# Optimization experiments

Hardware: AMD Instinct MI355X
Metric: run time of the kernel (lower is better)

The kernel has to match this reference:

```python
import jax, jax.numpy as jnp
import numpy as np

B, N, EMB = 64, 2048, 128
K1 = 3
L = EMB - K1 + 1            # 126, width after conv1/conv2
K2 = L // 2 + 1             # 64, conv3 kernel width -> conv3 out width = K2 - 1 = 63


def _conv_relu(x, w, b):
    # x: [M, 1, H, W]; w: [O, 1, kh, kw]; VALID conv + bias + relu
    y = jax.lax.conv_general_dilated(
        x, w, window_strides=(1, 1), padding='VALID',
        dimension_numbers=('NCHW', 'OIHW', 'NCHW'))
    return jax.nn.relu(y + b[None, :, None, None])


def _score(pairs, W1, b1, W2, b2, W3, b3, fw1, fb1, fw2, fb2, fw3, fb3):
    # pairs: [M, 2, D] -> score [M]
    x = pairs[:, None]                                  # [M,1,2,D]
    c1 = _conv_relu(x, W1, b1)                          # [M,1,2,L]
    c2 = _conv_relu(x, W2, b2)                          # [M,1,1,L]
    c = jnp.concatenate([c1, c2], axis=2)               # [M,1,3,L]
    c3 = _conv_relu(c, W3, b3)                          # [M,1,1,K2-1]
    h = c3.reshape(c3.shape[0], -1)                     # [M,K2-1]
    h = h @ fw1.T + fb1                                 # [M,K2//4]
    h = h @ fw2.T + fb2                                 # [M,16]
    h = h @ fw3.T + fb3                                 # [M,1]
    return h[:, 0]


def setup_inputs() -> dict:
    key = jax.random.key(0)
    ks = jax.random.split(key, 12)
    users = jax.random.normal(ks[0], (B, N, EMB), jnp.float32)
    top_user = jax.random.normal(ks[1], (B, EMB), jnp.float32)
    question = jax.random.normal(ks[2], (B, EMB), jnp.float32)
    # ragged valid-lengths: uids nonzero for first `len` entries, zero after
    lengths = jax.random.randint(ks[3], (B,), 1, N + 1)
    vals = jax.random.randint(ks[4], (B, N), 1, 10000)
    uids = jnp.where(jnp.arange(N)[None, :] < lengths[:, None], vals, 0).astype(jnp.int64)
    s = 0.1
    return {
        'users': users, 'top_user': top_user, 'question': question, 'uids': uids,
        'W1': jax.random.normal(ks[5], (1, 1, 1, K1), jnp.float32) * s,
        'b1': jnp.zeros((1,), jnp.float32),
        'W2': jax.random.normal(ks[6], (1, 1, 2, K1), jnp.float32) * s,
        'b2': jnp.zeros((1,), jnp.float32),
        'W3': jax.random.normal(ks[7], (1, 1, 3, K2), jnp.float32) * s,
        'b3': jnp.zeros((1,), jnp.float32),
        'fw1': jax.random.normal(ks[8], (K2 // 4, K2 - 1), jnp.float32) * s,
        'fb1': jnp.zeros((K2 // 4,), jnp.float32),
        'fw2': jax.random.normal(ks[9], (16, K2 // 4), jnp.float32) * s,
        'fb2': jnp.zeros((16,), jnp.float32),
        'fw3': jax.random.normal(ks[10], (1, 16), jnp.float32) * s,
        'fb3': jnp.zeros((1,), jnp.float32),
    }


def reference(users, top_user, question, uids,
              W1, b1, W2, b2, W3, b3, fw1, fb1, fw2, fb2, fw3, fb3):
    b, n, d = users.shape
    params = (W1, b1, W2, b2, W3, b3, fw1, fb1, fw2, fb2, fw3, fb3)
    # low-rank pairs: (candidate user, question) for every candidate slot
    q = jnp.broadcast_to(question[:, None], (b, n, d))
    low = jnp.stack([users, q], axis=2).reshape(b * n, 2, d)      # [B*N,2,D]
    high = jnp.stack([top_user, question], axis=1)                # [B,2,D]
    low_s = _score(low, *params).reshape(b, n)                    # [B,N]
    high_s = _score(high, *params)                                # [B]
    # ragged length = index of first zero uid (torch loop breaks there)
    is_zero = uids == 0
    cnt = jnp.where(jnp.any(is_zero, axis=1), jnp.argmax(is_zero, axis=1), n)
    mask = (jnp.arange(n)[None, :] < cnt[:, None]).astype(low_s.dtype)
    return jnp.sum(jax.nn.sigmoid(low_s - high_s[:, None]) * mask)
```

## Files before the change

### kernel.cpp

```cpp
#include <hip/hip_runtime.h>
#include <hip/hip_bf16.h>

typedef __attribute__((ext_vector_type(8))) short short8v;
typedef __attribute__((ext_vector_type(4))) float float4v;

#define NB 64
#define NN 2048
#define ED 128
#define GRID_P 1024

#define WS_WEFF  0
#define WS_BEFF  64
#define WS_SHIGH 128
#define WS_QTERM 192
#define WS_QPRE  (192+4096)
#define WS_BPACK (192+4096+8192)

static __device__ __forceinline__ unsigned int packbf2(float a, float b) {
    __hip_bfloat162 h = __float22bfloat162_rn(make_float2(a, b));
    return *(unsigned int*)&h;
}

__global__ __launch_bounds__(64) void k_prep(
    const float* __restrict__ top_user, const float* __restrict__ question,
    const float* __restrict__ W1, const float* __restrict__ b1,
    const float* __restrict__ W2, const float* __restrict__ b2,
    const float* __restrict__ W3, const float* __restrict__ b3,
    const float* __restrict__ fw1, const float* __restrict__ fb1,
    const float* __restrict__ fw2, const float* __restrict__ fb2,
    const float* __restrict__ fw3, const float* __restrict__ fb3,
    float* __restrict__ ws, float* __restrict__ out)
{
    const int lane = threadIdx.x;
    const int blk = blockIdx.x;
    __shared__ float g[16];
    __shared__ float w3s[192];
    w3s[lane] = W3[lane];
    w3s[64 + lane] = W3[64 + lane];
    w3s[128 + lane] = W3[128 + lane];
    if (lane < 16) {
        float s = 0.f;
        #pragma unroll
        for (int i = 0; i < 16; ++i) s += fw3[i] * fw2[i*16 + lane];
        g[lane] = s;
    }
    __syncthreads();

    if (blk >= NB) {
        const int kt = blk - NB;
        if (kt == 0) {
            if (lane == 0) out[0] = 0.f;
            float wv = 0.f;
            if (lane < 63) {
                #pragma unroll
                for (int k = 0; k < 16; ++k) wv += g[k] * fw1[k*63 + lane];
            }
            ws[WS_WEFF + lane] = wv;
            if (lane == 0) {
                float be = fb3[0];
                #pragma unroll
                for (int i = 0; i < 16; ++i) be += fw3[i] * fb2[i];
                #pragma unroll
                for (int k = 0; k < 16; ++k) be += g[k] * fb1[k];
                ws[WS_BEFF] = be;
            }
        }
        __hip_bfloat16* bp = (__hip_bfloat16*)(ws + WS_BPACK);
        const int g8 = (lane >> 4) * 8, li = lane & 15;
        #pragma unroll
        for (int nt = 0; nt < 4; ++nt) {
            const int tt = nt*16 + li;
            #pragma unroll
            for (int idx = 0; idx < 8; ++idx) {
                const int k = kt*32 + g8 + idx;
                const int j = k - tt;
                const int k2 = k - 128, j2 = k2 - tt;
                const bool v0 = (tt < 63) && (k < 126) && (j >= 0) && (j < 64);
                const bool v2 = (tt < 63) && (k2 >= 0) && (k2 < 126) && (j2 >= 0) && (j2 < 64);
                float v = (v0 ? w3s[j & 63] : 0.f) + (v2 ? w3s[128 + (j2 & 63)] : 0.f);
                bp[((kt*4 + nt)*64 + lane)*8 + idx] = __float2bfloat16(v);
            }
        }
        return;
    }

    float wv = 0.f;
    if (lane < 63) {
        #pragma unroll
        for (int k = 0; k < 16; ++k) wv += g[k] * fw1[k*63 + lane];
    }
    float be = fb3[0];
    #pragma unroll
    for (int i = 0; i < 16; ++i) be += fw3[i] * fb2[i];
    #pragma unroll
    for (int k = 0; k < 16; ++k) be += g[k] * fb1[k];

    __shared__ float q[132], tu[132], c1q[128], qt[64];
    __shared__ float4 D4[64];
    const int b = blk;
    ((float2*)q)[lane]  = ((const float2*)(question + b*ED))[lane];
    ((float2*)tu)[lane] = ((const float2*)(top_user + b*ED))[lane];
    if (lane == 63) {
        q[128]=0.f; q[129]=0.f; q[130]=0.f; q[131]=0.f;
        tu[128]=0.f; tu[129]=0.f; tu[130]=0.f; tu[131]=0.f;
    }
    __syncthreads();
    const float w10=W1[0], w11=W1[1], w12=W1[2];
    const float w20=W2[0], w21=W2[1], w22=W2[2];
    const float w23=W2[3], w24=W2[4], w25=W2[5];
    const float b1v=b1[0], b2v=b2[0], b3v=b3[0];
    const int i = 2*lane;
    float c1qa = fmaxf(b1v + w10*q[i]   + w11*q[i+1] + w12*q[i+2], 0.f);
    float c1qb = fmaxf(b1v + w10*q[i+1] + w11*q[i+2] + w12*q[i+3], 0.f);
    float qpa  = w23*q[i]   + w24*q[i+1] + w25*q[i+2];
    float qpb  = w23*q[i+1] + w24*q[i+2] + w25*q[i+3];
    float c1ta = fmaxf(b1v + w10*tu[i]   + w11*tu[i+1] + w12*tu[i+2], 0.f);
    float c1tb = fmaxf(b1v + w10*tu[i+1] + w11*tu[i+2] + w12*tu[i+3], 0.f);
    float c2a  = fmaxf(b2v + w20*tu[i]   + w21*tu[i+1] + w22*tu[i+2] + qpa, 0.f);
    float c2b  = fmaxf(b2v + w20*tu[i+1] + w21*tu[i+2] + w22*tu[i+3] + qpb, 0.f);
    if (lane == 63) { c1qa=0.f; c1qb=0.f; qpa=0.f; qpb=0.f; c1ta=0.f; c1tb=0.f; c2a=0.f; c2b=0.f; }
    c1q[i] = c1qa; c1q[i+1] = c1qb;
    ws[WS_QPRE + b*128 + i]     = qpa;
    ws[WS_QPRE + b*128 + i + 1] = qpb;
    D4[lane] = make_float4(c1ta, c2a, c1tb, c2b);
    __syncthreads();
    float qtv = 0.f;
    if (lane < 63) {
        #pragma unroll
        for (int j = 0; j < 64; ++j) qtv += w3s[64 + j] * c1q[lane + j];
    }
    qt[lane] = qtv;
    ws[WS_QTERM + b*64 + lane] = qtv + b3v;
    __syncthreads();
    float acc0 = b3v + qt[lane];
    float acc1 = 0.f;
    const float2* D2 = (const float2*)D4;
    #pragma unroll
    for (int j = 0; j < 64; ++j) {
        const float2 d = D2[lane + j];
        acc0 = fmaf(w3s[j],       d.x, acc0);
        acc1 = fmaf(w3s[128 + j], d.y, acc1);
    }
    float v = wv * fmaxf(acc0 + acc1, 0.f);
    #pragma unroll
    for (int off = 32; off > 0; off >>= 1) v += __shfl_xor(v, off, 64);
    if (lane == 0) ws[WS_SHIGH + b] = v + be;
}

__global__ __launch_bounds__(256) void k_pairs(
    const float* __restrict__ users, const int* __restrict__ uids,
    float* __restrict__ ws, float* __restrict__ out,
    const float* __restrict__ W1, const float* __restrict__ b1,
    const float* __restrict__ W2, const float* __restrict__ b2)
{
    __shared__ __align__(16) unsigned int X[64][132];
    __shared__ float pscore[2][2][64];
    const int tid = threadIdx.x;
    const int w = tid >> 6, lane = tid & 63;
    const int bid = blockIdx.x;
    const int b = bid >> 4;
    const int cpair = bid & 15;
    const int base0 = b*NN + cpair*128;
    const int base1 = base0 + 64;

    if (uids[base0] == 0) return;
    const bool act1 = (uids[base1] != 0);

    const int g = lane >> 4, li = lane & 15;
    const int nhalf = w >> 1;
    const int mbase = (w & 1) * 32;

    const int myuid0 = (w == 0) ? uids[base0 + lane] : 1;
    const int myuid1 = (w == 0) ? uids[base1 + lane] : 1;

    const float w10=W1[0], w11=W1[1], w12=W1[2];
    const float w20=W2[0], w21=W2[1], w22=W2[2];
    const float b1v=b1[0], b2v=b2[0];
    const int h = lane >> 5, j = lane & 31;
    const int r0 = w * 16;

    float4 u0r[8], u1r[8];
    #pragma unroll
    for (int pass = 0; pass < 8; ++pass) {
        const int r = r0 + pass*2 + h;
        u0r[pass] = *(const float4*)(users + (size_t)(base0 + r)*ED + 4*j);
        u1r[pass] = *(const float4*)(users + (size_t)(base1 + r)*ED + 4*j);
    }

    const __hip_bfloat16* bp = (const __hip_bfloat16*)(ws + WS_BPACK);
    short8v bfr0[8], bfr1[8];
    #pragma unroll
    for (int kt = 0; kt < 8; ++kt) {
        bfr0[kt] = *(const short8v*)(bp + (((kt*4 + nhalf*2 + 0)*64 + lane) << 3));
        bfr1[kt] = *(const short8v*)(bp + (((kt*4 + nhalf*2 + 1)*64 + lane) << 3));
    }

    const int t0 = nhalf*32 + li, t1 = t0 + 16;
    const float wf0 = ws[WS_WEFF + t0], wf1 = ws[WS_WEFF + t1];
    const float qt0 = ws[WS_QTERM + b*64 + t0], qt1 = ws[WS_QTERM + b*64 + t1];
    const float shigh = ws[WS_SHIGH + b], beff = ws[WS_BEFF];
    const float4 qp4 = *(const float4*)&ws[WS_QPRE + b*128 + 4*j];

    auto prep = [&](const float4* ur) {
        #pragma unroll
        for (int pass = 0; pass < 8; ++pass) {
            const int r = r0 + pass*2 + h;
            const float4 uu = ur[pass];
            const float nx = __shfl(uu.x, (lane + 1) & 63, 64);
            const float ny = __shfl(uu.y, (lane + 1) & 63, 64);
            float c10 = fmaxf(b1v + w10*uu.x + w11*uu.y + w12*uu.z, 0.f);
            float c11 = fmaxf(b1v + w10*uu.y + w11*uu.z + w12*uu.w, 0.f);
            float c12 = fmaxf(b1v + w10*uu.z + w11*uu.w + w12*nx  , 0.f);
            float c13 = fmaxf(b1v + w10*uu.w + w11*nx   + w12*ny  , 0.f);
            float c20 = fmaxf(b2v + w20*uu.x + w21*uu.y + w22*uu.z + qp4.x, 0.f);
            float c21 = fmaxf(b2v + w20*uu.y + w21*uu.z + w22*uu.w + qp4.y, 0.f);
            float c22 = fmaxf(b2v + w20*uu.z + w21*uu.w + w22*nx   + qp4.z, 0.f);
            float c23 = fmaxf(b2v + w20*uu.w + w21*nx   + w22*ny   + qp4.w, 0.f);
            if (j == 31) { c12 = 0.f; c13 = 0.f; c22 = 0.f; c23 = 0.f; }
            uint2 v1; v1.x = packbf2(c10, c11); v1.y = packbf2(c12, c13);
            uint2 v2; v2.x = packbf2(c20, c21); v2.y = packbf2(c22, c23);
            *(uint2*)&X[r][2*j]      = v1;
            *(uint2*)&X[r][64 + 2*j] = v2;
        }
    };

    auto gemm_ep = [&](int c) {
        float4v acc00 = {0.f,0.f,0.f,0.f}, acc01 = {0.f,0.f,0.f,0.f};
        float4v acc10 = {0.f,0.f,0.f,0.f}, acc11 = {0.f,0.f,0.f,0.f};
        const char* Xb = (const char*)&X[0][0];
        #pragma unroll
        for (int kt = 0; kt < 8; ++kt) {
            const short8v a0 = *(const short8v*)(Xb + (mbase + li)*528      + kt*64 + g*16);
            const short8v a1 = *(const short8v*)(Xb + (mbase + 16 + li)*528 + kt*64 + g*16);
            acc00 = __builtin_amdgcn_mfma_f32_16x16x32_bf16(a0, bfr0[kt], acc00, 0, 0, 0);
            acc01 = __builtin_amdgcn_mfma_f32_16x16x32_bf16(a0, bfr1[kt], acc01, 0, 0, 0);
            acc10 = __builtin_amdgcn_mfma_f32_16x16x32_bf16(a1, bfr0[kt], acc10, 0, 0, 0);
            acc11 = __builtin_amdgcn_mfma_f32_16x16x32_bf16(a1, bfr1[kt], acc11, 0, 0, 0);
        }
        #pragma unroll
        for (int mi = 0; mi < 2; ++mi) {
            #pragma unroll
            for (int reg = 0; reg < 4; ++reg) {
                const float a0v = mi ? acc10[reg] : acc00[reg];
                const float a1v = mi ? acc11[reg] : acc01[reg];
                float v = wf0 * fmaxf(a0v + qt0, 0.f) + wf1 * fmaxf(a1v + qt1, 0.f);
                v += __shfl_xor(v, 1, 64);
                v += __shfl_xor(v, 2, 64);
                v += __shfl_xor(v, 4, 64);
                v += __shfl_xor(v, 8, 64);
                if (li == 0) pscore[c][nhalf][mbase + mi*16 + g*4 + reg] = v;
            }
        }
    };

    prep(u0r);
    __syncthreads();
    gemm_ep(0);
    __syncthreads();
    if (act1) prep(u1r);
    __syncthreads();
    if (act1) gemm_ep(1);
    __syncthreads();

    if (w == 0) {
        const float d0 = pscore[0][0][lane] + pscore[0][1][lane] + beff - shigh;
        float val = (myuid0 != 0) ? 1.f / (1.f + __expf(-d0)) : 0.f;
        if (act1) {
            const float d1 = pscore[1][0][lane] + pscore[1][1][lane] + beff - shigh;
            val += (myuid1 != 0) ? 1.f / (1.f + __expf(-d1)) : 0.f;
        }
        #pragma unroll
        for (int off = 32; off > 0; off >>= 1) val += __shfl_xor(val, off, 64);
        if (lane == 0) atomicAdd(out, val);
    }
}

extern "C" void kernel_launch(void* const* d_in, const int* in_sizes, int n_in,
                              void* d_out, int out_size, void* d_ws, size_t ws_size,
                              hipStream_t stream)
{
    const float* users    = (const float*)d_in[0];
    const float* top_user = (const float*)d_in[1];
    const float* question = (const float*)d_in[2];
    const int*   uids     = (const int*)d_in[3];
    const float* W1  = (const float*)d_in[4];
    const float* b1  = (const float*)d_in[5];
    const float* W2  = (const float*)d_in[6];
    const float* b2  = (const float*)d_in[7];
    const float* W3  = (const float*)d_in[8];
    const float* b3  = (const float*)d_in[9];
    const float* fw1 = (const float*)d_in[10];
    const float* fb1 = (const float*)d_in[11];
    const float* fw2 = (const float*)d_in[12];
    const float* fb2 = (const float*)d_in[13];
    const float* fw3 = (const float*)d_in[14];
    const float* fb3 = (const float*)d_in[15];
    float* ws  = (float*)d_ws;
    float* out = (float*)d_out;

    hipLaunchKernelGGL(k_prep, dim3(NB + 8), dim3(64), 0, stream,
                       top_user, question, W1, b1, W2, b2, W3, b3,
                       fw1, fb1, fw2, fb2, fw3, fb3, ws, out);
    hipLaunchKernelGGL(k_pairs, dim3(GRID_P), dim3(256), 0, stream,
                       users, uids, ws, out, W1, b1, W2, b2);
}
```

Baseline: 31.74 us.

## Compact active 64-row chunks via prefix sum and launch one chunk per block

k_prep now counts, for each batch row, how many 64-candidate chunks begin with a nonzero uid and writes the counts to workspace. k_pairs runs a wave-level prefix scan over these counts, so each block maps to exactly one active chunk and inactive blocks exit early. This replaces the old fixed mapping of two chunks per block, which left blocks idle on padded rows and underused the GPU. The cost is a per-block scan over the 64 counts and a grid sized for the worst case, with excess blocks returning immediately.

```diff
diff --git a/kernel.cpp b/kernel.cpp
--- a/kernel.cpp
+++ b/kernel.cpp
@@ -7,7 +7,7 @@
 #define NB 64
 #define NN 2048
 #define ED 128
-#define GRID_P 1024
+#define GRID_P 2048
 
 #define WS_WEFF  0
 #define WS_BEFF  64
@@ -15,6 +15,7 @@
 #define WS_QTERM 192
 #define WS_QPRE  (192+4096)
 #define WS_BPACK (192+4096+8192)
+#define WS_QCNT  (WS_BPACK+8192)
 
 static __device__ __forceinline__ unsigned int packbf2(float a, float b) {
     __hip_bfloat162 h = __float22bfloat162_rn(make_float2(a, b));
@@ -29,10 +30,15 @@
     const float* __restrict__ fw1, const float* __restrict__ fb1,
     const float* __restrict__ fw2, const float* __restrict__ fb2,
     const float* __restrict__ fw3, const float* __restrict__ fb3,
+    const int* __restrict__ uids,
     float* __restrict__ ws, float* __restrict__ out)
 {
     const int lane = threadIdx.x;
     const int blk = blockIdx.x;
+
+    int act = 0;
+    if (blk < NB && lane < 32) act = (uids[blk*NN + lane*64] != 0) ? 1 : 0;
+
     __shared__ float g[16];
     __shared__ float w3s[192];
     w3s[lane] = W3[lane];
@@ -84,6 +90,11 @@
         return;
     }
 
+    {
+        const unsigned long long bm = __ballot(act);
+        if (lane == 0) ((int*)(ws + WS_QCNT))[blk] = (int)__popcll(bm);
+    }
+
     float wv = 0.f;
     if (lane < 63) {
         #pragma unroll
@@ -154,88 +165,93 @@
     const float* __restrict__ W2, const float* __restrict__ b2)
 {
     __shared__ __align__(16) unsigned int X[64][132];
-    __shared__ float pscore[2][2][64];
+    __shared__ float pscore[2][64];
     const int tid = threadIdx.x;
     const int w = tid >> 6, lane = tid & 63;
     const int bid = blockIdx.x;
-    const int b = bid >> 4;
-    const int cpair = bid & 15;
-    const int base0 = b*NN + cpair*128;
-    const int base1 = base0 + 64;
-
-    if (uids[base0] == 0) return;
-    const bool act1 = (uids[base1] != 0);
-
-    const int g = lane >> 4, li = lane & 15;
+
+    const int* qcnti = (const int*)(ws + WS_QCNT);
+    int incl = qcnti[lane];
+    #pragma unroll
+    for (int off = 1; off < 64; off <<= 1) {
+        const int t = __shfl_up(incl, off, 64);
+        if (lane >= off) incl += t;
+    }
+    const int total = __shfl(incl, 63, 64);
+    if (bid >= total) return;
+
+    const unsigned long long mm = __ballot(incl <= bid);
+    const int b0 = (int)__popcll(mm);
+    const int prefb = (b0 > 0) ? __shfl(incl, b0 - 1, 64) : 0;
+    const int pa0 = b0*NN + (bid - prefb)*64;
+
+    const int gfr = lane >> 4, li = lane & 15;
     const int nhalf = w >> 1;
     const int mbase = (w & 1) * 32;
-
-    const int myuid0 = (w == 0) ? uids[base0 + lane] : 1;
-    const int myuid1 = (w == 0) ? uids[base1 + lane] : 1;
+    const int h = lane >> 5, j = lane & 31;
+    const int r0 = w * 16;
+
+    float4 bufA[8];
+    #pragma unroll
+    for (int pass = 0; pass < 8; ++pass) {
+        const int r = r0 + pass*2 + h;
+        bufA[pass] = *(const float4*)(users + (size_t)(pa0 + r)*ED + 4*j);
+    }
+    const int m0 = (w == 0) ? uids[pa0 + lane] : 1;
+
+    const __hip_bfloat16* bp = (const __hip_bfloat16*)(ws + WS_BPACK);
+    short8v bfr0[8], bfr1[8];
+    #pragma unroll
+    for (int kt = 0; kt < 8; ++kt) {
+        bfr0[kt] = *(const short8v*)(bp + (((kt*4 + nhalf*2 + 0)*64 + lane) << 3));
+        bfr1[kt] = *(const short8v*)(bp + (((kt*4 + nhalf*2 + 1)*64 + lane) << 3));
+    }
+
+    const int t0 = nhalf*32 + li, t1 = t0 + 16;
+    const float wf0 = ws[WS_WEFF + t0], wf1 = ws[WS_WEFF + t1];
+    const float beff = ws[WS_BEFF];
+    const float qta0 = ws[WS_QTERM + b0*64 + t0], qtb0 = ws[WS_QTERM + b0*64 + t1];
+    const float sh0 = ws[WS_SHIGH + b0];
+    const float4 qp0 = *(const float4*)&ws[WS_QPRE + b0*128 + 4*j];
 
     const float w10=W1[0], w11=W1[1], w12=W1[2];
     const float w20=W2[0], w21=W2[1], w22=W2[2];
     const float b1v=b1[0], b2v=b2[0];
-    const int h = lane >> 5, j = lane & 31;
-    const int r0 = w * 16;
-
-    float4 u0r[8], u1r[8];
+
     #pragma unroll
     for (int pass = 0; pass < 8; ++pass) {
         const int r = r0 + pass*2 + h;
-        u0r[pass] = *(const float4*)(users + (size_t)(base0 + r)*ED + 4*j);
-        u1r[pass] = *(const float4*)(users + (size_t)(base1 + r)*ED + 4*j);
-    }
-
-    const __hip_bfloat16* bp = (const __hip_bfloat16*)(ws + WS_BPACK);
-    short8v bfr0[8], bfr1[8];
-    #pragma unroll
-    for (int kt = 0; kt < 8; ++kt) {
-        bfr0[kt] = *(const short8v*)(bp + (((kt*4 + nhalf*2 + 0)*64 + lane) << 3));
-        bfr1[kt] = *(const short8v*)(bp + (((kt*4 + nhalf*2 + 1)*64 + lane) << 3));
-    }
-
-    const int t0 = nhalf*32 + li, t1 = t0 + 16;
-    const float wf0 = ws[WS_WEFF + t0], wf1 = ws[WS_WEFF + t1];
-    const float qt0 = ws[WS_QTERM + b*64 + t0], qt1 = ws[WS_QTERM + b*64 + t1];
-    const float shigh = ws[WS_SHIGH + b], beff = ws[WS_BEFF];
-    const float4 qp4 = *(const float4*)&ws[WS_QPRE + b*128 + 4*j];
-
-    auto prep = [&](const float4* ur) {
-        #pragma unroll
-        for (int pass = 0; pass < 8; ++pass) {
-            const int r = r0 + pass*2 + h;
-            const float4 uu = ur[pass];
-            const float nx = __shfl(uu.x, (lane + 1) & 63, 64);
-            const float ny = __shfl(uu.y, (lane + 1) & 63, 64);
-            float c10 = fmaxf(b1v + w10*uu.x + w11*uu.y + w12*uu.z, 0.f);
-            float c11 = fmaxf(b1v + w10*uu.y + w11*uu.z + w12*uu.w, 0.f);
-            float c12 = fmaxf(b1v + w10*uu.z + w11*uu.w + w12*nx  , 0.f);
-            float c13 = fmaxf(b1v + w10*uu.w + w11*nx   + w12*ny  , 0.f);
-            float c20 = fmaxf(b2v + w20*uu.x + w21*uu.y + w22*uu.z + qp4.x, 0.f);
-            float c21 = fmaxf(b2v + w20*uu.y + w21*uu.z + w22*uu.w + qp4.y, 0.f);
-            float c22 = fmaxf(b2v + w20*uu.z + w21*uu.w + w22*nx   + qp4.z, 0.f);
-            float c23 = fmaxf(b2v + w20*uu.w + w21*nx   + w22*ny   + qp4.w, 0.f);
-            if (j == 31) { c12 = 0.f; c13 = 0.f; c22 = 0.f; c23 = 0.f; }
-            uint2 v1; v1.x = packbf2(c10, c11); v1.y = packbf2(c12, c13);
-            uint2 v2; v2.x = packbf2(c20, c21); v2.y = packbf2(c22, c23);
-            *(uint2*)&X[r][2*j]      = v1;
-            *(uint2*)&X[r][64 + 2*j] = v2;
-        }
-    };
-
-    auto gemm_ep = [&](int c) {
+        const float4 uu = bufA[pass];
+        const float nx = __shfl(uu.x, (lane + 1) & 63, 64);
+        const float ny = __shfl(uu.y, (lane + 1) & 63, 64);
+        float c10 = fmaxf(b1v + w10*uu.x + w11*uu.y + w12*uu.z, 0.f);
+        float c11 = fmaxf(b1v + w10*uu.y + w11*uu.z + w12*uu.w, 0.f);
+        float c12 = fmaxf(b1v + w10*uu.z + w11*uu.w + w12*nx  , 0.f);
+        float c13 = fmaxf(b1v + w10*uu.w + w11*nx   + w12*ny  , 0.f);
+        float c20 = fmaxf(b2v + w20*uu.x + w21*uu.y + w22*uu.z + qp0.x, 0.f);
+        float c21 = fmaxf(b2v + w20*uu.y + w21*uu.z + w22*uu.w + qp0.y, 0.f);
+        float c22 = fmaxf(b2v + w20*uu.z + w21*uu.w + w22*nx   + qp0.z, 0.f);
+        float c23 = fmaxf(b2v + w20*uu.w + w21*nx   + w22*ny   + qp0.w, 0.f);
+        if (j == 31) { c12 = 0.f; c13 = 0.f; c22 = 0.f; c23 = 0.f; }
+        uint2 v1; v1.x = packbf2(c10, c11); v1.y = packbf2(c12, c13);
+        uint2 v2; v2.x = packbf2(c20, c21); v2.y = packbf2(c22, c23);
+        *(uint2*)&X[r][2*j]      = v1;
+        *(uint2*)&X[r][64 + 2*j] = v2;
+    }
+    __syncthreads();
+
+    {
         float4v acc00 = {0.f,0.f,0.f,0.f}, acc01 = {0.f,0.f,0.f,0.f};
         float4v acc10 = {0.f,0.f,0.f,0.f}, acc11 = {0.f,0.f,0.f,0.f};
         const char* Xb = (const char*)&X[0][0];
         #pragma unroll
         for (int kt = 0; kt < 8; ++kt) {
-            const short8v a0 = *(const short8v*)(Xb + (mbase + li)*528      + kt*64 + g*16);
-            const short8v a1 = *(const short8v*)(Xb + (mbase + 16 + li)*528 + kt*64 + g*16);
-            acc00 = __builtin_amdgcn_mfma_f32_16x16x32_bf16(a0, bfr0[kt], acc00, 0, 0, 0);
-            acc01 = __builtin_amdgcn_mfma_f32_16x16x32_bf16(a0, bfr1[kt], acc01, 0, 0, 0);
-            acc10 = __builtin_amdgcn_mfma_f32_16x16x32_bf16(a1, bfr0[kt], acc10, 0, 0, 0);
-            acc11 = __builtin_amdgcn_mfma_f32_16x16x32_bf16(a1, bfr1[kt], acc11, 0, 0, 0);
+            const short8v aa0 = *(const short8v*)(Xb + (mbase + li)*528      + kt*64 + gfr*16);
+            const short8v aa1 = *(const short8v*)(Xb + (mbase + 16 + li)*528 + kt*64 + gfr*16);
+            acc00 = __builtin_amdgcn_mfma_f32_16x16x32_bf16(aa0, bfr0[kt], acc00, 0, 0, 0);
+            acc01 = __builtin_amdgcn_mfma_f32_16x16x32_bf16(aa0, bfr1[kt], acc01, 0, 0, 0);
+            acc10 = __builtin_amdgcn_mfma_f32_16x16x32_bf16(aa1, bfr0[kt], acc10, 0, 0, 0);
+            acc11 = __builtin_amdgcn_mfma_f32_16x16x32_bf16(aa1, bfr1[kt], acc11, 0, 0, 0);
         }
         #pragma unroll
         for (int mi = 0; mi < 2; ++mi) {
@@ -243,32 +259,20 @@
             for (int reg = 0; reg < 4; ++reg) {
                 const float a0v = mi ? acc10[reg] : acc00[reg];
                 const float a1v = mi ? acc11[reg] : acc01[reg];
-                float v = wf0 * fmaxf(a0v + qt0, 0.f) + wf1 * fmaxf(a1v + qt1, 0.f);
+                float v = wf0 * fmaxf(a0v + qta0, 0.f) + wf1 * fmaxf(a1v + qtb0, 0.f);
                 v += __shfl_xor(v, 1, 64);
                 v += __shfl_xor(v, 2, 64);
                 v += __shfl_xor(v, 4, 64);
                 v += __shfl_xor(v, 8, 64);
-                if (li == 0) pscore[c][nhalf][mbase + mi*16 + g*4 + reg] = v;
+                if (li == 0) pscore[nhalf][mbase + mi*16 + gfr*4 + reg] = v;
             }
         }
-    };
-
-    prep(u0r);
-    __syncthreads();
-    gemm_ep(0);
-    __syncthreads();
-    if (act1) prep(u1r);
-    __syncthreads();
-    if (act1) gemm_ep(1);
+    }
     __syncthreads();
 
     if (w == 0) {
-        const float d0 = pscore[0][0][lane] + pscore[0][1][lane] + beff - shigh;
-        float val = (myuid0 != 0) ? 1.f / (1.f + __expf(-d0)) : 0.f;
-        if (act1) {
-            const float d1 = pscore[1][0][lane] + pscore[1][1][lane] + beff - shigh;
-            val += (myuid1 != 0) ? 1.f / (1.f + __expf(-d1)) : 0.f;
-        }
+        const float d = pscore[0][lane] + pscore[1][lane] + beff - sh0;
+        float val = (m0 != 0) ? 1.f / (1.f + __expf(-d)) : 0.f;
         #pragma unroll
         for (int off = 32; off > 0; off >>= 1) val += __shfl_xor(val, off, 64);
         if (lane == 0) atomicAdd(out, val);
@@ -300,7 +304,7 @@
 
     hipLaunchKernelGGL(k_prep, dim3(NB + 8), dim3(64), 0, stream,
                        top_user, question, W1, b1, W2, b2, W3, b3,
-                       fw1, fb1, fw2, fb2, fw3, fb3, ws, out);
+                       fw1, fb1, fw2, fb2, fw3, fb3, uids, ws, out);
     hipLaunchKernelGGL(k_pairs, dim3(GRID_P), dim3(256), 0, stream,
                        users, uids, ws, out, W1, b1, W2, b2);
 }
```

Measured after the change: 32.06 us. No clear change (+1.0%).
